# Performance work log

Hardware: AMD Instinct MI355X
Metric: run time of the kernel (lower is better)

## Reference

```python
import jax, jax.numpy as jnp
import numpy as np

THRESHOLD = 1.5
MIN_AREA = 3
B, H, W = 8, 1024, 1024


def _label_components(mask):
    """8-connectivity connected-component labeling by min-index propagation.
    mask: [B,H,W] bool. Returns int32 labels [B,H,W]; each component is labeled
    by the minimum global flat index of its pixels; background pixels = B*H*W.
    Labels are globally unique across the batch (matches sort_labels' per-batch
    unique relabeling up to a label permutation).
    """
    N = B * H * W
    SENT = jnp.int32(N)
    flat = jnp.arange(N, dtype=jnp.int32).reshape(B, H, W)
    lab0 = jnp.where(mask, flat, SENT)

    def neighbor_min(lab):
        p = jnp.pad(lab, ((0, 0), (1, 1), (1, 1)), constant_values=N)
        m = lab
        for dr in (-1, 0, 1):
            for dc in (-1, 0, 1):
                if dr == 0 and dc == 0:
                    continue
                m = jnp.minimum(m, p[:, 1 + dr:1 + dr + H, 1 + dc:1 + dc + W])
        return jnp.where(mask, m, SENT)

    def cond(state):
        return state[1]

    def body(state):
        lab, _ = state
        new = neighbor_min(lab)
        return new, jnp.any(new != lab)

    lab, _ = jax.lax.while_loop(cond, body, (lab0, jnp.array(True)))
    return lab


def setup_inputs() -> dict:
    key = jax.random.key(0)
    x = jax.random.normal(key, (B, H, W // 1), dtype=jnp.float32)
    return {"input_tensor": x.reshape(B, 1, H, W)}


def reference(input_tensor):
    """Dense encoding of the original ragged output: for every pixel belonging
    to a cluster with area > MIN_AREA, emit the cluster's max value and the
    (row, col) of the first (lowest flat index) occurrence of that max;
    background / small-cluster pixels get (0, -1, -1). Since THRESHOLD > 0,
    max over masked_fill(0) in the original equals max over cluster pixels.
    """
    x = input_tensor[:, 0]                  # [B,H,W]
    N = B * H * W
    nseg = N + 1                            # last segment = background
    mask = (x >= THRESHOLD)
    ids = _label_components(mask).reshape(-1)          # [N] int32 in [0, N]
    vals = x.reshape(-1)
    fg = mask.reshape(-1)

    area = jax.ops.segment_sum(fg.astype(jnp.float32), ids, num_segments=nseg)
    cmax = jax.ops.segment_max(vals, ids, num_segments=nseg)

    within = jnp.tile(jnp.arange(H * W, dtype=jnp.int32), B)  # flat idx in image
    is_max = (vals == cmax[ids]) & fg
    cand = jnp.where(is_max, within, jnp.int32(H * W))
    amin = jax.ops.segment_min(cand, ids, num_segments=nseg)  # first argmax

    valid = fg & (area[ids] > MIN_AREA)
    out_max = jnp.where(valid, cmax[ids], jnp.float32(0.0)).reshape(B, H, W)
    aidx = amin[ids]
    row = jnp.where(valid, aidx // W, jnp.int32(-1)).reshape(B, H, W)
    col = jnp.where(valid, aidx % W, jnp.int32(-1)).reshape(B, H, W)
    return out_max, row, col
```

## Files before the change

kernel.cpp:

```cpp
#include <hip/hip_runtime.h>
#include <stdint.h>

#define THRESH 1.5f
constexpr int NPIX  = 8 * 1024 * 1024;
constexpr int HW    = 1024 * 1024;
constexpr int WW    = 1024;
constexpr int NWORD = NPIX / 32;
constexpr int WPR   = WW / 32;

constexpr int BLK     = 256;
constexpr int GRD_PX4 = NPIX / (BLK * 4);
constexpr int GRD_W   = NWORD / BLK;

constexpr int SPB_R      = 128;
constexpr int BASE_SLOTS = GRD_PX4 * SPB_R;
constexpr int OVF_SLOTS  = 16384;
constexpr int CAP        = BASE_SLOTS + OVF_SLOTS;
constexpr int ZINT4 = CAP * 12 / 16;
static_assert((CAP * 12) % 16 == 0, "zero region must be int4-divisible");
static_assert(ZINT4 <= GRD_PX4 * BLK, "mask_init must cover the zero region");

constexpr int WLSTRIDE = 1024;

__device__ __forceinline__ int find_root(const int* __restrict__ P, int x) {
    int p = P[x];
    while (p != x && p < NPIX) { x = p; p = P[x]; }
    return x;
}

__device__ __forceinline__ void merge(int* P, int a, int b) {
    int ra = find_root(P, a);
    int rb = find_root(P, b);
    while (ra != rb) {
        if (ra < rb) { int t = ra; ra = rb; rb = t; }
        int old = atomicCAS(&P[ra], ra, rb);
        if (old == ra) break;
        ra = find_root(P, old);
        rb = find_root(P, rb);
    }
}

__global__ void mask_init_k(const float* __restrict__ x, int* __restrict__ parent,
                            unsigned* __restrict__ mask, uint2* __restrict__ wl,
                            int* __restrict__ wl_cnt, int4* __restrict__ zbase,
                            int* __restrict__ ovf) {
    __shared__ unsigned s_nib[BLK];
    __shared__ int s_rank;
    int t  = threadIdx.x;
    int gt = blockIdx.x * BLK + t;
    if (gt < ZINT4) zbase[gt] = make_int4(0, 0, 0, 0);
    int i4 = gt * 4;
    float4 v = *(const float4*)(x + i4);
    unsigned nib = (unsigned)(v.x >= THRESH) | ((unsigned)(v.y >= THRESH) << 1) |
                   ((unsigned)(v.z >= THRESH) << 2) | ((unsigned)(v.w >= THRESH) << 3);
    *(int4*)(parent + i4) = make_int4(i4, i4 + 1, i4 + 2, i4 + 3);
    if (t == 0) s_rank = 0;
    s_nib[t] = nib;
    __syncthreads();
    if ((t & 7) == 0) {
        unsigned w = 0;
        #pragma unroll
        for (int k = 0; k < 8; k++) w |= s_nib[t + k] << (4 * k);
        mask[gt >> 3] = w;
    }
    int nfg = __popc(nib);
    if (nfg) {
        int r = atomicAdd(&s_rank, nfg);
        uint2* dst = wl + (size_t)blockIdx.x * WLSTRIDE;
        if (nib & 1u) dst[r++] = make_uint2((unsigned)i4,     __float_as_uint(v.x));
        if (nib & 2u) dst[r++] = make_uint2((unsigned)i4 + 1, __float_as_uint(v.y));
        if (nib & 4u) dst[r++] = make_uint2((unsigned)i4 + 2, __float_as_uint(v.z));
        if (nib & 8u) dst[r++] = make_uint2((unsigned)i4 + 3, __float_as_uint(v.w));
    }
    __syncthreads();
    if (t == 0) wl_cnt[blockIdx.x] = s_rank;
    if (gt == 0) *ovf = 0;
}

__global__ void union_k(const unsigned* __restrict__ mask, int* __restrict__ parent) {
    int w = blockIdx.x * BLK + threadIdx.x;
    unsigned cur = mask[w];
    if (!cur) return;
    int r  = (w >> 5) & (WW - 1);
    int cw = w & (WPR - 1);
    unsigned prev = (cw > 0) ? mask[w - 1] : 0u;
    unsigned above = 0u, abovePrev = 0u, aboveNext = 0u;
    if (r > 0) {
        above     = mask[w - WPR];
        abovePrev = (cw > 0)       ? mask[w - WPR - 1] : 0u;
        aboveNext = (cw < WPR - 1) ? mask[w - WPR + 1] : 0u;
    }
    int base = w << 5;
    unsigned mW  = cur & ((cur   << 1) | (prev      >> 31));
    unsigned mN  = cur & above;
    unsigned mNW = cur & ((above << 1) | (abovePrev >> 31));
    unsigned mNE = cur & ((above >> 1) | ((aboveNext & 1u) << 31));
    while (mW)  { int b = __ffs(mW)  - 1; mW  &= mW  - 1; merge(parent, base + b, base + b - 1); }
    while (mN)  { int b = __ffs(mN)  - 1; mN  &= mN  - 1; merge(parent, base + b, base + b - WW); }
    while (mNW) { int b = __ffs(mNW) - 1; mNW &= mNW - 1; merge(parent, base + b, base + b - WW - 1); }
    while (mNE) { int b = __ffs(mNE) - 1; mNE &= mNE - 1; merge(parent, base + b, base + b - WW + 1); }
}

__global__ void cstats_k(const uint2* __restrict__ wl, const int* __restrict__ wl_cnt,
                         int* __restrict__ parent, int* __restrict__ cnt,
                         unsigned long long* __restrict__ best,
                         int* __restrict__ ovf) {
    __shared__ int s_cnt;
    if (threadIdx.x == 0) s_cnt = 0;
    __syncthreads();
    int region = blockIdx.x;
    int c = wl_cnt[region];
    const uint2* src = wl + (size_t)region * WLSTRIDE;
    for (int j = threadIdx.x; j < c; j += 64) {
        uint2 e = src[j];
        int p = (int)e.x;
        int cid;
        int xn = p;
        while (true) {
            int pe = parent[xn];
            if (pe >= NPIX) { cid = pe - NPIX; break; }
            if (pe == xn) {
                int rank = atomicAdd(&s_cnt, 1);
                int slot;
                if (rank < SPB_R) slot = region * SPB_R + rank;
                else { int o2 = atomicAdd(ovf, 1);
                       slot = BASE_SLOTS + (o2 < OVF_SLOTS ? o2 : OVF_SLOTS - 1); }
                int old = atomicCAS(&parent[xn], xn, NPIX + slot);
                if (old == xn)    { cid = slot; break; }
                if (old >= NPIX)  { cid = old - NPIX; break; }
                xn = old;
            } else {
                xn = pe;
            }
        }
        parent[p] = NPIX + cid;
        atomicAdd(&cnt[cid], 1);
        unsigned within = (unsigned)(p & (HW - 1));
        unsigned long long pk =
            ((unsigned long long)e.y << 32) | (unsigned long long)(~within);
        atomicMax(&best[cid], pk);
    }
}

__device__ __forceinline__ void lookup_one(const int* __restrict__ parent,
                                           const int* __restrict__ cnt,
                                           const unsigned long long* __restrict__ best,
                                           int p, float& om, float& orow, float& ocol) {
    int cid = parent[p] - NPIX;
    if (cid >= 0 && cid < CAP && cnt[cid] > 3) {
        unsigned long long pk = best[cid];
        om   = __uint_as_float((unsigned)(pk >> 32));
        unsigned idx = ~((unsigned)pk);
        orow = (float)(idx >> 10);
        ocol = (float)(idx & (WW - 1));
    }
}

__global__ void out_k(const unsigned* __restrict__ mask, const int* __restrict__ parent,
                      const int* __restrict__ cnt,
                      const unsigned long long* __restrict__ best,
                      float* __restrict__ o) {
    int t = blockIdx.x * BLK + threadIdx.x;
    unsigned nib = (mask[t >> 3] >> ((t & 7) * 4)) & 0xFu;
    int i4 = t * 4;
    float4 m  = make_float4(0.f, 0.f, 0.f, 0.f);
    float4 rr = make_float4(-1.f, -1.f, -1.f, -1.f);
    float4 cc = make_float4(-1.f, -1.f, -1.f, -1.f);
    if (nib) {
        if (nib & 1u) lookup_one(parent, cnt, best, i4,     m.x, rr.x, cc.x);
        if (nib & 2u) lookup_one(parent, cnt, best, i4 + 1, m.y, rr.y, cc.y);
        if (nib & 4u) lookup_one(parent, cnt, best, i4 + 2, m.z, rr.z, cc.z);
        if (nib & 8u) lookup_one(parent, cnt, best, i4 + 3, m.w, rr.w, cc.w);
    }
    *(float4*)(o + i4)            = m;
    *(float4*)(o + NPIX + i4)     = rr;
    *(float4*)(o + 2 * NPIX + i4) = cc;
}

extern "C" void kernel_launch(void* const* d_in, const int* in_sizes, int n_in,
                              void* d_out, int out_size, void* d_ws, size_t ws_size,
                              hipStream_t stream) {
    const float* x = (const float*)d_in[0];
    float* o = (float*)d_out;

    char* base = (char*)d_ws;
    int* parent = (int*)base;
    size_t off = (size_t)NPIX * 4;
    unsigned long long* best = (unsigned long long*)(base + off);
    int4* zbase = (int4*)(base + off);                             off += (size_t)CAP * 8;
    int* cnt       = (int*)(base + off);                           off += (size_t)CAP * 4;
    unsigned* mask = (unsigned*)(base + off);                      off += (size_t)NWORD * 4;
    int* wl_cnt    = (int*)(base + off);                           off += (size_t)GRD_PX4 * 4;
    uint2* wl      = (uint2*)(base + off);                         off += (size_t)GRD_PX4 * WLSTRIDE * 8;
    int* ovf       = (int*)(base + off);

    mask_init_k<<<GRD_PX4, BLK, 0, stream>>>(x, parent, mask, wl, wl_cnt, zbase, ovf);
    union_k    <<<GRD_W,   BLK, 0, stream>>>(mask, parent);
    cstats_k   <<<GRD_PX4, 64,  0, stream>>>(wl, wl_cnt, parent, cnt, best, ovf);
    out_k      <<<GRD_PX4, BLK, 0, stream>>>(mask, parent, cnt, best, o);
}
```

Before: 196.3 us.

## Pre-link horizontal runs in init and prune redundant vertical unions with path halving

Parent initialization now points each foreground pixel at the start of its horizontal run within the row, computed from the shared-memory row bitmask, so the union kernel no longer merges west neighbours. The union kernel skips row 0, drops diagonal merges already covered by a direct north link and keeps only the first north link per vertical run segment, cutting atomic CAS merges. find_root now does path halving with writes, which adds stores but shortens later traversals. A risk is that find_root no longer stops at labels >= NPIX, so it relies on those labels never being present during union.

```diff
diff --git a/kernel.cpp b/kernel.cpp
--- a/kernel.cpp
+++ b/kernel.cpp
@@ -22,9 +22,14 @@
 
 constexpr int WLSTRIDE = 1024;
 
-__device__ __forceinline__ int find_root(const int* __restrict__ P, int x) {
+
+__device__ __forceinline__ int find_root(int* __restrict__ P, int x) {
     int p = P[x];
-    while (p != x && p < NPIX) { x = p; p = P[x]; }
+    while (p != x) {
+        int g = P[p];
+        if (g != p) P[x] = g;
+        x = p; p = g;
+    }
     return x;
 }
 
@@ -45,6 +50,7 @@
                             int* __restrict__ wl_cnt, int4* __restrict__ zbase,
                             int* __restrict__ ovf) {
     __shared__ unsigned s_nib[BLK];
+    __shared__ unsigned s_word[WPR];
     __shared__ int s_rank;
     int t  = threadIdx.x;
     int gt = blockIdx.x * BLK + t;
@@ -53,7 +59,6 @@
     float4 v = *(const float4*)(x + i4);
     unsigned nib = (unsigned)(v.x >= THRESH) | ((unsigned)(v.y >= THRESH) << 1) |
                    ((unsigned)(v.z >= THRESH) << 2) | ((unsigned)(v.w >= THRESH) << 3);
-    *(int4*)(parent + i4) = make_int4(i4, i4 + 1, i4 + 2, i4 + 3);
     if (t == 0) s_rank = 0;
     s_nib[t] = nib;
     __syncthreads();
@@ -61,8 +66,40 @@
         unsigned w = 0;
         #pragma unroll
         for (int k = 0; k < 8; k++) w |= s_nib[t + k] << (4 * k);
+        s_word[t >> 3] = w;
         mask[gt >> 3] = w;
     }
+    __syncthreads();
+
+    int rowstart = blockIdx.x << 10;
+    int r0 = t << 2;
+    int rs0 = 0, rs1 = 0, rs2 = 0, rs3 = 0;
+    if (nib & 1u) {
+        bool prevSet = (r0 != 0) &&
+            ((s_word[(r0 - 1) >> 5] >> ((r0 - 1) & 31)) & 1u);
+        if (!prevSet) rs0 = r0;
+        else {
+            int wI = r0 >> 5, b = r0 & 31;
+            unsigned notset = b ? (~s_word[wI] & ((1u << b) - 1)) : 0u;
+            int j = wI;
+            if (!notset) {
+                j = wI - 1;
+                while (j >= 0 && s_word[j] == 0xFFFFFFFFu) j--;
+                notset = (j >= 0) ? ~s_word[j] : 0u;
+            }
+            rs0 = (j < 0) ? 0 : (j * 32 + (31 - __clz(notset)) + 1);
+        }
+    }
+    if (nib & 2u) rs1 = (nib & 1u) ? rs0 : r0 + 1;
+    if (nib & 4u) rs2 = (nib & 2u) ? rs1 : r0 + 2;
+    if (nib & 8u) rs3 = (nib & 4u) ? rs2 : r0 + 3;
+    int4 pv;
+    pv.x = (nib & 1u) ? rowstart + rs0 : i4;
+    pv.y = (nib & 2u) ? rowstart + rs1 : i4 + 1;
+    pv.z = (nib & 4u) ? rowstart + rs2 : i4 + 2;
+    pv.w = (nib & 8u) ? rowstart + rs3 : i4 + 3;
+    *(int4*)(parent + i4) = pv;
+
     int nfg = __popc(nib);
     if (nfg) {
         int r = atomicAdd(&s_rank, nfg);
@@ -79,23 +116,22 @@
 
 __global__ void union_k(const unsigned* __restrict__ mask, int* __restrict__ parent) {
     int w = blockIdx.x * BLK + threadIdx.x;
+    int r = (w >> 5) & (WW - 1);
+    if (r == 0) return;
     unsigned cur = mask[w];
     if (!cur) return;
-    int r  = (w >> 5) & (WW - 1);
     int cw = w & (WPR - 1);
-    unsigned prev = (cw > 0) ? mask[w - 1] : 0u;
-    unsigned above = 0u, abovePrev = 0u, aboveNext = 0u;
-    if (r > 0) {
-        above     = mask[w - WPR];
-        abovePrev = (cw > 0)       ? mask[w - WPR - 1] : 0u;
-        aboveNext = (cw < WPR - 1) ? mask[w - WPR + 1] : 0u;
-    }
-    int base = w << 5;
-    unsigned mW  = cur & ((cur   << 1) | (prev      >> 31));
+    unsigned above     = mask[w - WPR];
+    unsigned abovePrev = (cw > 0)       ? mask[w - WPR - 1] : 0u;
+    unsigned aboveNext = (cw < WPR - 1) ? mask[w - WPR + 1] : 0u;
     unsigned mN  = cur & above;
     unsigned mNW = cur & ((above << 1) | (abovePrev >> 31));
     unsigned mNE = cur & ((above >> 1) | ((aboveNext & 1u) << 31));
-    while (mW)  { int b = __ffs(mW)  - 1; mW  &= mW  - 1; merge(parent, base + b, base + b - 1); }
+    mNW &= ~mN;
+    mNE &= ~mN;
+    mN  &= ~(mN << 1);
+    if (!(mN | mNW | mNE)) return;
+    int base = w << 5;
     while (mN)  { int b = __ffs(mN)  - 1; mN  &= mN  - 1; merge(parent, base + b, base + b - WW); }
     while (mNW) { int b = __ffs(mNW) - 1; mNW &= mNW - 1; merge(parent, base + b, base + b - WW - 1); }
     while (mNE) { int b = __ffs(mNE) - 1; mNE &= mNE - 1; merge(parent, base + b, base + b - WW + 1); }
```

After: 189.7 us. 3.3% less time.
